# Kernel tuning notes

Hardware: AMD Instinct MI355X
Metric: run time of the kernel (lower is better)

The kernel has to match this reference:

```python
import jax, jax.numpy as jnp
import numpy as np

S = 5            # num_species
B = 1_000_000    # batch (proteins)
D = 32           # input_dim == hidden_dim (hard-coded 32 in forward)
EPS = 1e-5       # torch BatchNorm1d default eps
BRANCH_WEIGHT = 0.92


def setup_inputs() -> dict:
    key = jax.random.key(0)
    ks = jax.random.split(key, 20)
    f32 = jnp.float32
    inp = {
        "network_feat": jax.random.normal(ks[0], (B, D), f32),
        "species_ids": jax.random.randint(ks[1], (B,), 0, S),
        # per-species params, stacked along species axis. Weights stored [in, out]
        # (transpose of torch nn.Linear layout) so y = x @ W + b.
        "W1": jax.random.normal(ks[2], (S, D, D), f32) * 0.1,
        "b1": jax.random.normal(ks[3], (S, D), f32) * 0.1,
        "bn1_gamma": jax.random.uniform(ks[4], (S, D), f32, 0.5, 1.5),
        "bn1_beta": jax.random.normal(ks[5], (S, D), f32) * 0.1,
        "bn1_mean": jax.random.normal(ks[6], (S, D), f32) * 0.1,
        "bn1_var": jax.random.uniform(ks[7], (S, D), f32, 0.5, 1.5),
        "W2": jax.random.normal(ks[8], (S, D, D), f32) * 0.1,
        "b2": jax.random.normal(ks[9], (S, D), f32) * 0.1,
        "bn2_gamma": jax.random.uniform(ks[10], (S, D), f32, 0.5, 1.5),
        "bn2_beta": jax.random.normal(ks[11], (S, D), f32) * 0.1,
        "bn2_mean": jax.random.normal(ks[12], (S, D), f32) * 0.1,
        "bn2_var": jax.random.uniform(ks[13], (S, D), f32, 0.5, 1.5),
        "Wsc": jax.random.normal(ks[14], (S, D, D), f32) * 0.1,
        "bsc": jax.random.normal(ks[15], (S, D), f32) * 0.1,
        "Wsh": jax.random.normal(ks[16], (D, D), f32) * 0.1,
        "bsh": jax.random.normal(ks[17], (D,), f32) * 0.1,
    }
    return inp


def _bn(h, gamma, beta, mean, var):
    # BatchNorm1d in eval mode: running-stat normalization + affine.
    return (h - mean) * jax.lax.rsqrt(var + EPS) * gamma + beta


def reference(network_feat, species_ids, W1, b1, bn1_gamma, bn1_beta, bn1_mean,
              bn1_var, W2, b2, bn2_gamma, bn2_beta, bn2_mean, bn2_var,
              Wsc, bsc, Wsh, bsh):
    # Eval mode: dropout = identity, BN uses running stats.
    # Instead of gather/scatter per species, compute each species' tiny MLP on the
    # full batch and select with the species mask (same math; dense & fusible).
    x = network_feat
    out = jnp.zeros_like(x)
    for s in range(S):  # small fixed expert count
        shortcut = x @ Wsc[s] + bsc[s]
        h = jax.nn.relu(x @ W1[s] + b1[s])
        h = _bn(h, bn1_gamma[s], bn1_beta[s], bn1_mean[s], bn1_var[s])
        h = jax.nn.relu(h @ W2[s] + b2[s] + shortcut)
        h = _bn(h, bn2_gamma[s], bn2_beta[s], bn2_mean[s], bn2_var[s])
        mask = (species_ids == s)[:, None]  # [B, 1]
        out = jnp.where(mask, h, out)
    out = jax.nn.relu(out @ Wsh + bsh)  # shared MLP (dropout inactive)
    return out * BRANCH_WEIGHT
```

## Files before the change

kernel.cpp:

```cpp
#include <hip/hip_runtime.h>


#define EPSBN 1e-5f
#define TPB 256
#define WIN 256
#define NBLKMAX 768

typedef __attribute__((ext_vector_type(8))) short bf16x8;
typedef __attribute__((ext_vector_type(16))) float f32x16;
typedef __attribute__((ext_vector_type(4))) unsigned u32x4;

union FU { unsigned u[4]; bf16x8 v; u32x4 q; };

static __device__ __forceinline__ unsigned pkbf(float lo, float hi) {
    unsigned r;
    asm("v_cvt_pk_bf16_f32 %0, %1, %2" : "=v"(r) : "v"(lo), "v"(hi));
    return r;
}

static __device__ __forceinline__ void ldsbar() {
    asm volatile("s_waitcnt lgkmcnt(0)" ::: "memory");
    __builtin_amdgcn_s_barrier();
}

__global__ void k_pre(unsigned* __restrict__ wfrag, float* __restrict__ bconst,
                      const float* __restrict__ W1, const float* __restrict__ b1,
                      const float* __restrict__ g1, const float* __restrict__ be1,
                      const float* __restrict__ mu1, const float* __restrict__ va1,
                      const float* __restrict__ W2, const float* __restrict__ b2,
                      const float* __restrict__ g2, const float* __restrict__ be2,
                      const float* __restrict__ mu2, const float* __restrict__ va2,
                      const float* __restrict__ Wsc, const float* __restrict__ bsc,
                      const float* __restrict__ Wsh, const float* __restrict__ bsh) {
    if (blockIdx.x < 40) {
        const int i = blockIdx.x * 256 + threadIdx.x;
        const int p = i & 3, l = (i >> 2) & 63, c = (i >> 8) & 1;
        const int m = (i >> 9) & 3, s = i >> 11;
        const int ln = l & 31, hi = l >> 5;
        const int k0 = c * 16 + hi * 8 + 2 * p;
        float lo, hv;
        if (m == 0)      { lo = W1[s*1024 + k0*32 + ln];  hv = W1[s*1024 + (k0+1)*32 + ln]; }
        else if (m == 1) { lo = Wsc[s*1024 + k0*32 + ln]; hv = Wsc[s*1024 + (k0+1)*32 + ln]; }
        else if (m == 2) {
            float A0 = g1[s*32+k0]   * rsqrtf(va1[s*32+k0]   + EPSBN);
            float A1 = g1[s*32+k0+1] * rsqrtf(va1[s*32+k0+1] + EPSBN);
            lo = A0 * W2[s*1024 + k0*32 + ln]; hv = A1 * W2[s*1024 + (k0+1)*32 + ln];
        } else {
            float A0 = 0.92f * g2[s*32+k0]   * rsqrtf(va2[s*32+k0]   + EPSBN);
            float A1 = 0.92f * g2[s*32+k0+1] * rsqrtf(va2[s*32+k0+1] + EPSBN);
            lo = A0 * Wsh[k0*32 + ln]; hv = A1 * Wsh[(k0+1)*32 + ln];
        }
        wfrag[i] = pkbf(lo, hv);
    } else {
        for (int i = threadIdx.x; i < 480; i += 256) {
            const int reg = i & 15, hi = (i >> 4) & 1, t = i >> 5;
            const int q = t % 3, s = t / 3;
            const int r = (reg & 3) + 8 * (reg >> 2) + 4 * hi;
            float v;
            if (q == 0) v = b1[s*32 + r];
            else if (q == 1) {
                v = b2[s*32 + r] + bsc[s*32 + r];
                for (int k = 0; k < 32; ++k) {
                    float A = g1[s*32+k] * rsqrtf(va1[s*32+k] + EPSBN);
                    float C = be1[s*32+k] - mu1[s*32+k] * A;
                    v = fmaf(C, W2[s*1024 + k*32 + r], v);
                }
            } else {
                v = bsh[r];
                for (int k = 0; k < 32; ++k) {
                    float A = g2[s*32+k] * rsqrtf(va2[s*32+k] + EPSBN);
                    float C = be2[s*32+k] - mu2[s*32+k] * A;
                    v = fmaf(C, Wsh[k*32 + r], v);
                }
                v *= 0.92f;
            }
            bconst[i] = v;
        }
    }
}

static __device__ __forceinline__ void reluT(const f32x16& c, bf16x8& f0, bf16x8& f1) {
    unsigned p[8];
    #pragma unroll
    for (int i = 0; i < 8; ++i)
        p[i] = pkbf(fmaxf(c[2 * i], 0.f), fmaxf(c[2 * i + 1], 0.f));
    auto s0 = __builtin_amdgcn_permlane32_swap(p[0], p[2], false, false);
    auto s1 = __builtin_amdgcn_permlane32_swap(p[1], p[3], false, false);
    auto s2 = __builtin_amdgcn_permlane32_swap(p[4], p[6], false, false);
    auto s3 = __builtin_amdgcn_permlane32_swap(p[5], p[7], false, false);
    FU u0, u1;
    u0.u[0] = s0[0]; u0.u[1] = s1[0]; u0.u[2] = s0[1]; u0.u[3] = s1[1];
    u1.u[0] = s2[0]; u1.u[1] = s3[0]; u1.u[2] = s2[1]; u1.u[3] = s3[1];
    f0 = u0.v; f1 = u1.v;
}

__global__ __launch_bounds__(TPB, 3) void k_main(
    const float* __restrict__ X, const int* __restrict__ sid,
    const unsigned* __restrict__ wfrag, const float* __restrict__ bconst,
    float* __restrict__ out, int B) {
    __shared__ __align__(16) unsigned char xb[16384];
    __shared__ __align__(16) float ob[8192];
    __shared__ float clds[480];
    __shared__ int idxl[416];
    __shared__ int wq[4][5];

    const int tid = threadIdx.x;
    const int l   = tid & 63;
    const int ln  = l & 31;
    const int hi  = l >> 5;
    const int wav = tid >> 6;
    const unsigned long long ltmask = (1ull << l) - 1ull;

    for (int i = tid; i < 480; i += TPB) clds[i] = bconst[i];

    const int nwin = (B + WIN - 1) / WIN;
    const long fmaxo = (long)B * 32 - 8;

    float4 pa[4], pb[4];
    int svp = -1;

    int w0 = blockIdx.x;
    if (w0 < nwin) {
        #pragma unroll
        for (int k = 0; k < 4; ++k) {
            long fo = (long)w0 * (WIN * 32) + k * 2048 + tid * 8;
            if (fo > fmaxo) fo = fmaxo;
            pa[k] = *(const float4*)(X + fo);
            pb[k] = *(const float4*)(X + fo + 4);
        }
        int row = w0 * WIN + tid;
        svp = (row < B) ? sid[row < B ? row : B - 1] : -1;
    }

    for (int w = w0; w < nwin; w += gridDim.x) {
        const int wbase = w * WIN;
        const int rows = min(WIN, B - wbase);

        #pragma unroll
        for (int k = 0; k < 4; ++k) {
            FU u;
            u.u[0] = pkbf(pa[k].x, pa[k].y); u.u[1] = pkbf(pa[k].z, pa[k].w);
            u.u[2] = pkbf(pb[k].x, pb[k].y); u.u[3] = pkbf(pb[k].z, pb[k].w);
            const int row  = k * 64 + (tid >> 2);
            const int slot = (tid & 3) ^ (row & 3);
            *(u32x4*)(xb + row * 64 + slot * 16) = u.q;
        }

        const int s = svp;
        int prank = 0;
        #pragma unroll
        for (int sp = 0; sp < 5; ++sp) {
            unsigned long long m = __ballot(s == sp);
            if (l == 0) wq[wav][sp] = (int)__popcll(m);
            if (s == sp) prank = (int)__popcll(m & ltmask);
        }
        for (int i = tid; i < 416; i += TPB) idxl[i] = -1;
        ldsbar();

        int tb[6];
        {
            int t = 0;
            #pragma unroll
            for (int sp = 0; sp < 5; ++sp) {
                tb[sp] = t;
                int c = wq[0][sp] + wq[1][sp] + wq[2][sp] + wq[3][sp];
                t += (c + 31) >> 5;
            }
            tb[5] = t;
        }
        if (s >= 0) {
            int off = tb[s] * 32 + prank;
            for (int w2 = 0; w2 < wav; ++w2) off += wq[w2][s];
            idxl[off] = tid;
        }

        const int wn = w + gridDim.x;
        if (wn < nwin) {
            #pragma unroll
            for (int k = 0; k < 4; ++k) {
                long fo = (long)wn * (WIN * 32) + k * 2048 + tid * 8;
                if (fo > fmaxo) fo = fmaxo;
                pa[k] = *(const float4*)(X + fo);
                pb[k] = *(const float4*)(X + fo + 4);
            }
            int row = wn * WIN + tid;
            svp = (row < B) ? sid[row] : -1;
        }
        ldsbar();

        const int ntl = tb[5];
        for (int t = wav; t < ntl; t += 4) {
            int csp = 0;
            #pragma unroll
            for (int k = 1; k < 5; ++k) csp += (t >= tb[k]) ? 1 : 0;
            csp = __builtin_amdgcn_readfirstlane(csp);
            const int lid = idxl[t * 32 + ln];
            const int r = lid < 0 ? 0 : lid;

            const unsigned* wp = wfrag + csp * 2048;
            FU w00, w01, w10, w11, w20, w21, w30, w31;
            w00.q = *(const u32x4*)(wp + (0 * 64 + l) * 4);
            w01.q = *(const u32x4*)(wp + (1 * 64 + l) * 4);
            w10.q = *(const u32x4*)(wp + (2 * 64 + l) * 4);
            w11.q = *(const u32x4*)(wp + (3 * 64 + l) * 4);
            w20.q = *(const u32x4*)(wp + (4 * 64 + l) * 4);
            w21.q = *(const u32x4*)(wp + (5 * 64 + l) * 4);
            w30.q = *(const u32x4*)(wp + (6 * 64 + l) * 4);
            w31.q = *(const u32x4*)(wp + (7 * 64 + l) * 4);

            const float* cp = clds + csp * 96;
            f32x16 a1 = *(const f32x16*)(cp + hi * 16);
            f32x16 a2 = *(const f32x16*)(cp + 32 + hi * 16);

            const int rs = r & 3;
            const bf16x8 b0 = *(const bf16x8*)(xb + r * 64 + ((hi ^ rs) << 4));
            const bf16x8 b1 = *(const bf16x8*)(xb + r * 64 + (((2 + hi) ^ rs) << 4));

            a1 = __builtin_amdgcn_mfma_f32_32x32x16_bf16(w00.v, b0, a1, 0, 0, 0);
            a2 = __builtin_amdgcn_mfma_f32_32x32x16_bf16(w10.v, b0, a2, 0, 0, 0);
            a1 = __builtin_amdgcn_mfma_f32_32x32x16_bf16(w01.v, b1, a1, 0, 0, 0);
            a2 = __builtin_amdgcn_mfma_f32_32x32x16_bf16(w11.v, b1, a2, 0, 0, 0);

            bf16x8 h0, h1;
            reluT(a1, h0, h1);
            a2 = __builtin_amdgcn_mfma_f32_32x32x16_bf16(w20.v, h0, a2, 0, 0, 0);
            a2 = __builtin_amdgcn_mfma_f32_32x32x16_bf16(w21.v, h1, a2, 0, 0, 0);

            bf16x8 g0, g1;
            reluT(a2, g0, g1);
            f32x16 a3 = *(const f32x16*)(cp + 64 + hi * 16);
            a3 = __builtin_amdgcn_mfma_f32_32x32x16_bf16(w30.v, g0, a3, 0, 0, 0);
            a3 = __builtin_amdgcn_mfma_f32_32x32x16_bf16(w31.v, g1, a3, 0, 0, 0);

            if (lid >= 0) {
                #pragma unroll
                for (int q = 0; q < 4; ++q) {
                    float4 v;
                    v.x = fmaxf(a3[4 * q + 0], 0.f);
                    v.y = fmaxf(a3[4 * q + 1], 0.f);
                    v.z = fmaxf(a3[4 * q + 2], 0.f);
                    v.w = fmaxf(a3[4 * q + 3], 0.f);
                    const int fs = (hi * 4 + q * 8) ^ ((lid & 7) << 2);
                    *(float4*)(ob + lid * 32 + fs) = v;
                }
            }
        }
        ldsbar();

        #pragma unroll
        for (int k = 0; k < 8; ++k) {
            const int p = k * TPB + tid;
            const int row = p >> 3, sl = p & 7;
            if (row < rows) {
                const int fs = (sl * 4) ^ ((row & 7) << 2);
                float4 v = *(const float4*)(ob + row * 32 + fs);
                *(float4*)(out + (long)(wbase + row) * 32 + sl * 4) = v;
            }
        }
    }
}

extern "C" void kernel_launch(void* const* d_in, const int* in_sizes, int n_in,
                              void* d_out, int out_size, void* d_ws, size_t ws_size,
                              hipStream_t stream) {
    const float* X   = (const float*)d_in[0];
    const int*   sid = (const int*)d_in[1];
    const float* W1  = (const float*)d_in[2];
    const float* b1  = (const float*)d_in[3];
    const float* g1  = (const float*)d_in[4];
    const float* be1 = (const float*)d_in[5];
    const float* mu1 = (const float*)d_in[6];
    const float* va1 = (const float*)d_in[7];
    const float* W2  = (const float*)d_in[8];
    const float* b2  = (const float*)d_in[9];
    const float* g2  = (const float*)d_in[10];
    const float* be2 = (const float*)d_in[11];
    const float* mu2 = (const float*)d_in[12];
    const float* va2 = (const float*)d_in[13];
    const float* Wsc = (const float*)d_in[14];
    const float* bsc = (const float*)d_in[15];
    const float* Wsh = (const float*)d_in[16];
    const float* bsh = (const float*)d_in[17];
    float* out = (float*)d_out;
    const int B = in_sizes[1];

    unsigned* wfrag = (unsigned*)d_ws;
    float* bconst   = (float*)(wfrag + 10240);

    k_pre<<<41, 256, 0, stream>>>(wfrag, bconst,
                                  W1, b1, g1, be1, mu1, va1,
                                  W2, b2, g2, be2, mu2, va2,
                                  Wsc, bsc, Wsh, bsh);

    const int nwin = (B + WIN - 1) / WIN;
    const int nblocks = min(NBLKMAX, nwin);
    k_main<<<nblocks, TPB, 0, stream>>>(X, sid, wfrag, bconst, out, B);
}
```

Before: 63.66 us.

## Drop LDS output staging, store final MFMA results directly, raise occupancy

The last shared-MLP MFMA now swaps its operands so the result comes out transposed: each lane holds one output feature for 16 rows. The kernel writes straight to global memory using the row indices kept in LDS, which removes the 32KB output staging buffer and its barrier-and-copy phase. Freeing that LDS lets launch bounds rise from 3 to 5 blocks per SM and the grid cap rise to 1792 blocks. A per-species bias vector is added to the precomputed constants. The direct stores are scattered 4-byte writes: each lane writes to a different row, which may coalesce worse than the old float4 row copies.

```diff
diff --git a/kernel.cpp b/kernel.cpp
--- a/kernel.cpp
+++ b/kernel.cpp
@@ -4,7 +4,7 @@
 #define EPSBN 1e-5f
 #define TPB 256
 #define WIN 256
-#define NBLKMAX 768
+#define NBLKMAX 1792
 
 typedef __attribute__((ext_vector_type(8))) short bf16x8;
 typedef __attribute__((ext_vector_type(16))) float f32x16;
@@ -73,6 +73,7 @@
                     v = fmaf(C, Wsh[k*32 + r], v);
                 }
                 v *= 0.92f;
+                bconst[480 + s * 32 + r] = v;
             }
             bconst[i] = v;
         }
@@ -94,13 +95,12 @@
     f0 = u0.v; f1 = u1.v;
 }
 
-__global__ __launch_bounds__(TPB, 3) void k_main(
+__global__ __launch_bounds__(TPB, 5) void k_main(
     const float* __restrict__ X, const int* __restrict__ sid,
     const unsigned* __restrict__ wfrag, const float* __restrict__ bconst,
     float* __restrict__ out, int B) {
     __shared__ __align__(16) unsigned char xb[16384];
-    __shared__ __align__(16) float ob[8192];
-    __shared__ float clds[480];
+    __shared__ float clds[640];
     __shared__ int idxl[416];
     __shared__ int wq[4][5];
 
@@ -111,7 +111,7 @@
     const int wav = tid >> 6;
     const unsigned long long ltmask = (1ull << l) - 1ull;
 
-    for (int i = tid; i < 480; i += TPB) clds[i] = bconst[i];
+    for (int i = tid; i < 640; i += TPB) clds[i] = bconst[i];
 
     const int nwin = (B + WIN - 1) / WIN;
     const long fmaxo = (long)B * 32 - 8;
@@ -119,7 +119,7 @@
     float4 pa[4], pb[4];
     int svp = -1;
 
-    int w0 = blockIdx.x;
+    const int w0 = blockIdx.x;
     if (w0 < nwin) {
         #pragma unroll
         for (int k = 0; k < 4; ++k) {
@@ -128,13 +128,14 @@
             pa[k] = *(const float4*)(X + fo);
             pb[k] = *(const float4*)(X + fo + 4);
         }
-        int row = w0 * WIN + tid;
-        svp = (row < B) ? sid[row < B ? row : B - 1] : -1;
+        const int row = w0 * WIN + tid;
+        svp = (row < B) ? sid[row] : -1;
     }
 
     for (int w = w0; w < nwin; w += gridDim.x) {
         const int wbase = w * WIN;
-        const int rows = min(WIN, B - wbase);
+
+        ldsbar();
 
         #pragma unroll
         for (int k = 0; k < 4; ++k) {
@@ -183,7 +184,7 @@
                 pa[k] = *(const float4*)(X + fo);
                 pb[k] = *(const float4*)(X + fo + 4);
             }
-            int row = wn * WIN + tid;
+            const int row = wn * WIN + tid;
             svp = (row < B) ? sid[row] : -1;
         }
         ldsbar();
@@ -228,33 +229,20 @@
 
             bf16x8 g0, g1;
             reluT(a2, g0, g1);
-            f32x16 a3 = *(const f32x16*)(cp + 64 + hi * 16);
-            a3 = __builtin_amdgcn_mfma_f32_32x32x16_bf16(w30.v, g0, a3, 0, 0, 0);
-            a3 = __builtin_amdgcn_mfma_f32_32x32x16_bf16(w31.v, g1, a3, 0, 0, 0);
-
-            if (lid >= 0) {
-                #pragma unroll
-                for (int q = 0; q < 4; ++q) {
-                    float4 v;
-                    v.x = fmaxf(a3[4 * q + 0], 0.f);
-                    v.y = fmaxf(a3[4 * q + 1], 0.f);
-                    v.z = fmaxf(a3[4 * q + 2], 0.f);
-                    v.w = fmaxf(a3[4 * q + 3], 0.f);
-                    const int fs = (hi * 4 + q * 8) ^ ((lid & 7) << 2);
-                    *(float4*)(ob + lid * 32 + fs) = v;
-                }
-            }
-        }
-        ldsbar();
-
-        #pragma unroll
-        for (int k = 0; k < 8; ++k) {
-            const int p = k * TPB + tid;
-            const int row = p >> 3, sl = p & 7;
-            if (row < rows) {
-                const int fs = (sl * 4) ^ ((row & 7) << 2);
-                float4 v = *(const float4*)(ob + row * 32 + fs);
-                *(float4*)(out + (long)(wbase + row) * 32 + sl * 4) = v;
+
+            const float bsh_n = clds[480 + csp * 32 + ln];
+            f32x16 a3;
+            #pragma unroll
+            for (int rr = 0; rr < 16; ++rr) a3[rr] = bsh_n;
+            a3 = __builtin_amdgcn_mfma_f32_32x32x16_bf16(g0, w30.v, a3, 0, 0, 0);
+            a3 = __builtin_amdgcn_mfma_f32_32x32x16_bf16(g1, w31.v, a3, 0, 0, 0);
+
+            #pragma unroll
+            for (int reg = 0; reg < 16; ++reg) {
+                const int si = (reg & 3) + 8 * (reg >> 2) + 4 * hi;
+                const int lid2 = idxl[t * 32 + si];
+                if (lid2 >= 0)
+                    out[(long)(wbase + lid2) * 32 + ln] = fmaxf(a3[reg], 0.f);
             }
         }
     }
```

After: 111.4 us. 1.75x slower.

## Fuse weight preprocessing into main kernel, stage weights in LDS, bf16 output staging

Applied to the files above, without the earlier changes.

Removes the separate preprocessing kernel and has every block build the packed bf16 weight fragments and folded bias constants directly into shared memory. The per-tile weight fragment loads then come from LDS instead of global memory. Output staging in LDS switches from fp32 to packed bf16, and the grid shrinks to 512 blocks with 2 blocks per CU. This saves one kernel launch and its dependency, at the cost of redundant per-block preprocessing (including serial 32-step bias loops) and bf16 rounding of the final output.

```diff
diff --git a/kernel.cpp b/kernel.cpp
--- a/kernel.cpp
+++ b/kernel.cpp
@@ -4,11 +4,12 @@
 #define EPSBN 1e-5f
 #define TPB 256
 #define WIN 256
-#define NBLKMAX 768
+#define NBLK 512
 
 typedef __attribute__((ext_vector_type(8))) short bf16x8;
 typedef __attribute__((ext_vector_type(16))) float f32x16;
 typedef __attribute__((ext_vector_type(4))) unsigned u32x4;
+typedef __attribute__((ext_vector_type(2))) unsigned u32x2;
 
 union FU { unsigned u[4]; bf16x8 v; u32x4 q; };
 
@@ -21,62 +22,6 @@
 static __device__ __forceinline__ void ldsbar() {
     asm volatile("s_waitcnt lgkmcnt(0)" ::: "memory");
     __builtin_amdgcn_s_barrier();
-}
-
-__global__ void k_pre(unsigned* __restrict__ wfrag, float* __restrict__ bconst,
-                      const float* __restrict__ W1, const float* __restrict__ b1,
-                      const float* __restrict__ g1, const float* __restrict__ be1,
-                      const float* __restrict__ mu1, const float* __restrict__ va1,
-                      const float* __restrict__ W2, const float* __restrict__ b2,
-                      const float* __restrict__ g2, const float* __restrict__ be2,
-                      const float* __restrict__ mu2, const float* __restrict__ va2,
-                      const float* __restrict__ Wsc, const float* __restrict__ bsc,
-                      const float* __restrict__ Wsh, const float* __restrict__ bsh) {
-    if (blockIdx.x < 40) {
-        const int i = blockIdx.x * 256 + threadIdx.x;
-        const int p = i & 3, l = (i >> 2) & 63, c = (i >> 8) & 1;
-        const int m = (i >> 9) & 3, s = i >> 11;
-        const int ln = l & 31, hi = l >> 5;
-        const int k0 = c * 16 + hi * 8 + 2 * p;
-        float lo, hv;
-        if (m == 0)      { lo = W1[s*1024 + k0*32 + ln];  hv = W1[s*1024 + (k0+1)*32 + ln]; }
-        else if (m == 1) { lo = Wsc[s*1024 + k0*32 + ln]; hv = Wsc[s*1024 + (k0+1)*32 + ln]; }
-        else if (m == 2) {
-            float A0 = g1[s*32+k0]   * rsqrtf(va1[s*32+k0]   + EPSBN);
-            float A1 = g1[s*32+k0+1] * rsqrtf(va1[s*32+k0+1] + EPSBN);
-            lo = A0 * W2[s*1024 + k0*32 + ln]; hv = A1 * W2[s*1024 + (k0+1)*32 + ln];
-        } else {
-            float A0 = 0.92f * g2[s*32+k0]   * rsqrtf(va2[s*32+k0]   + EPSBN);
-            float A1 = 0.92f * g2[s*32+k0+1] * rsqrtf(va2[s*32+k0+1] + EPSBN);
-            lo = A0 * Wsh[k0*32 + ln]; hv = A1 * Wsh[(k0+1)*32 + ln];
-        }
-        wfrag[i] = pkbf(lo, hv);
-    } else {
-        for (int i = threadIdx.x; i < 480; i += 256) {
-            const int reg = i & 15, hi = (i >> 4) & 1, t = i >> 5;
-            const int q = t % 3, s = t / 3;
-            const int r = (reg & 3) + 8 * (reg >> 2) + 4 * hi;
-            float v;
-            if (q == 0) v = b1[s*32 + r];
-            else if (q == 1) {
-                v = b2[s*32 + r] + bsc[s*32 + r];
-                for (int k = 0; k < 32; ++k) {
-                    float A = g1[s*32+k] * rsqrtf(va1[s*32+k] + EPSBN);
-                    float C = be1[s*32+k] - mu1[s*32+k] * A;
-                    v = fmaf(C, W2[s*1024 + k*32 + r], v);
-                }
-            } else {
-                v = bsh[r];
-                for (int k = 0; k < 32; ++k) {
-                    float A = g2[s*32+k] * rsqrtf(va2[s*32+k] + EPSBN);
-                    float C = be2[s*32+k] - mu2[s*32+k] * A;
-                    v = fmaf(C, Wsh[k*32 + r], v);
-                }
-                v *= 0.92f;
-            }
-            bconst[i] = v;
-        }
-    }
 }
 
 static __device__ __forceinline__ void reluT(const f32x16& c, bf16x8& f0, bf16x8& f1) {
@@ -94,12 +39,20 @@
     f0 = u0.v; f1 = u1.v;
 }
 
-__global__ __launch_bounds__(TPB, 3) void k_main(
+__global__ __launch_bounds__(TPB, 2) void k_main(
     const float* __restrict__ X, const int* __restrict__ sid,
-    const unsigned* __restrict__ wfrag, const float* __restrict__ bconst,
+    const float* __restrict__ W1, const float* __restrict__ b1,
+    const float* __restrict__ g1, const float* __restrict__ be1,
+    const float* __restrict__ mu1, const float* __restrict__ va1,
+    const float* __restrict__ W2, const float* __restrict__ b2,
+    const float* __restrict__ g2, const float* __restrict__ be2,
+    const float* __restrict__ mu2, const float* __restrict__ va2,
+    const float* __restrict__ Wsc, const float* __restrict__ bsc,
+    const float* __restrict__ Wsh, const float* __restrict__ bsh,
     float* __restrict__ out, int B) {
+    __shared__ __align__(16) unsigned wlds[10240];
     __shared__ __align__(16) unsigned char xb[16384];
-    __shared__ __align__(16) float ob[8192];
+    __shared__ __align__(16) unsigned obh[4096];
     __shared__ float clds[480];
     __shared__ int idxl[416];
     __shared__ int wq[4][5];
@@ -111,15 +64,12 @@
     const int wav = tid >> 6;
     const unsigned long long ltmask = (1ull << l) - 1ull;
 
-    for (int i = tid; i < 480; i += TPB) clds[i] = bconst[i];
-
     const int nwin = (B + WIN - 1) / WIN;
     const long fmaxo = (long)B * 32 - 8;
 
     float4 pa[4], pb[4];
     int svp = -1;
-
-    int w0 = blockIdx.x;
+    const int w0 = blockIdx.x;
     if (w0 < nwin) {
         #pragma unroll
         for (int k = 0; k < 4; ++k) {
@@ -128,8 +78,52 @@
             pa[k] = *(const float4*)(X + fo);
             pb[k] = *(const float4*)(X + fo + 4);
         }
-        int row = w0 * WIN + tid;
-        svp = (row < B) ? sid[row < B ? row : B - 1] : -1;
+        const int row = w0 * WIN + tid;
+        svp = (row < B) ? sid[row] : -1;
+    }
+
+    for (int i = tid; i < 10240; i += TPB) {
+        const int p = i & 3, L = (i >> 2) & 63, c = (i >> 8) & 1;
+        const int m = (i >> 9) & 3, s = i >> 11;
+        const int LN = L & 31, HI = L >> 5;
+        const int k0 = c * 16 + HI * 8 + 2 * p;
+        float lo, hv;
+        if (m == 0)      { lo = W1[s*1024 + k0*32 + LN];  hv = W1[s*1024 + (k0+1)*32 + LN]; }
+        else if (m == 1) { lo = Wsc[s*1024 + k0*32 + LN]; hv = Wsc[s*1024 + (k0+1)*32 + LN]; }
+        else if (m == 2) {
+            float A0 = g1[s*32+k0]   * rsqrtf(va1[s*32+k0]   + EPSBN);
+            float A1 = g1[s*32+k0+1] * rsqrtf(va1[s*32+k0+1] + EPSBN);
+            lo = A0 * W2[s*1024 + k0*32 + LN]; hv = A1 * W2[s*1024 + (k0+1)*32 + LN];
+        } else {
+            float A0 = 0.92f * g2[s*32+k0]   * rsqrtf(va2[s*32+k0]   + EPSBN);
+            float A1 = 0.92f * g2[s*32+k0+1] * rsqrtf(va2[s*32+k0+1] + EPSBN);
+            lo = A0 * Wsh[k0*32 + LN]; hv = A1 * Wsh[(k0+1)*32 + LN];
+        }
+        wlds[i] = pkbf(lo, hv);
+    }
+    for (int i = tid; i < 480; i += TPB) {
+        const int reg = i & 15, HI = (i >> 4) & 1, t = i >> 5;
+        const int q = t % 3, s = t / 3;
+        const int r = (reg & 3) + 8 * (reg >> 2) + 4 * HI;
+        float v;
+        if (q == 0) v = b1[s*32 + r];
+        else if (q == 1) {
+            v = b2[s*32 + r] + bsc[s*32 + r];
+            for (int k = 0; k < 32; ++k) {
+                float A = g1[s*32+k] * rsqrtf(va1[s*32+k] + EPSBN);
+                float C = be1[s*32+k] - mu1[s*32+k] * A;
+                v = fmaf(C, W2[s*1024 + k*32 + r], v);
+            }
+        } else {
+            v = bsh[r];
+            for (int k = 0; k < 32; ++k) {
+                float A = g2[s*32+k] * rsqrtf(va2[s*32+k] + EPSBN);
+                float C = be2[s*32+k] - mu2[s*32+k] * A;
+                v = fmaf(C, Wsh[k*32 + r], v);
+            }
+            v *= 0.92f;
+        }
+        clds[i] = v;
     }
 
     for (int w = w0; w < nwin; w += gridDim.x) {
@@ -183,7 +177,7 @@
                 pa[k] = *(const float4*)(X + fo);
                 pb[k] = *(const float4*)(X + fo + 4);
             }
-            int row = wn * WIN + tid;
+            const int row = wn * WIN + tid;
             svp = (row < B) ? sid[row] : -1;
         }
         ldsbar();
@@ -197,7 +191,7 @@
             const int lid = idxl[t * 32 + ln];
             const int r = lid < 0 ? 0 : lid;
 
-            const unsigned* wp = wfrag + csp * 2048;
+            const unsigned* wp = wlds + csp * 2048;
             FU w00, w01, w10, w11, w20, w21, w30, w31;
             w00.q = *(const u32x4*)(wp + (0 * 64 + l) * 4);
             w01.q = *(const u32x4*)(wp + (1 * 64 + l) * 4);
@@ -235,13 +229,11 @@
             if (lid >= 0) {
                 #pragma unroll
                 for (int q = 0; q < 4; ++q) {
-                    float4 v;
-                    v.x = fmaxf(a3[4 * q + 0], 0.f);
-                    v.y = fmaxf(a3[4 * q + 1], 0.f);
-                    v.z = fmaxf(a3[4 * q + 2], 0.f);
-                    v.w = fmaxf(a3[4 * q + 3], 0.f);
-                    const int fs = (hi * 4 + q * 8) ^ ((lid & 7) << 2);
-                    *(float4*)(ob + lid * 32 + fs) = v;
+                    unsigned u0 = pkbf(fmaxf(a3[4 * q + 0], 0.f), fmaxf(a3[4 * q + 1], 0.f));
+                    unsigned u1 = pkbf(fmaxf(a3[4 * q + 2], 0.f), fmaxf(a3[4 * q + 3], 0.f));
+                    const int off = (4 * q + 2 * hi) ^ ((lid & 7) << 1);
+                    u32x2 uu; uu[0] = u0; uu[1] = u1;
+                    *(u32x2*)(obh + lid * 16 + off) = uu;
                 }
             }
         }
@@ -252,8 +244,13 @@
             const int p = k * TPB + tid;
             const int row = p >> 3, sl = p & 7;
             if (row < rows) {
-                const int fs = (sl * 4) ^ ((row & 7) << 2);
-                float4 v = *(const float4*)(ob + row * 32 + fs);
+                const int off = (sl * 2) ^ ((row & 7) << 1);
+                u32x2 uu = *(const u32x2*)(obh + row * 16 + off);
+                float4 v;
+                v.x = __uint_as_float(uu[0] << 16);
+                v.y = __uint_as_float(uu[0] & 0xffff0000u);
+                v.z = __uint_as_float(uu[1] << 16);
+                v.w = __uint_as_float(uu[1] & 0xffff0000u);
                 *(float4*)(out + (long)(wbase + row) * 32 + sl * 4) = v;
             }
         }
@@ -284,15 +281,10 @@
     float* out = (float*)d_out;
     const int B = in_sizes[1];
 
-    unsigned* wfrag = (unsigned*)d_ws;
-    float* bconst   = (float*)(wfrag + 10240);
-
-    k_pre<<<41, 256, 0, stream>>>(wfrag, bconst,
-                                  W1, b1, g1, be1, mu1, va1,
-                                  W2, b2, g2, be2, mu2, va2,
-                                  Wsc, bsc, Wsh, bsh);
-
     const int nwin = (B + WIN - 1) / WIN;
-    const int nblocks = min(NBLKMAX, nwin);
-    k_main<<<nblocks, TPB, 0, stream>>>(X, sid, wfrag, bconst, out, B);
-}
+    const int nblocks = min(NBLK, nwin);
+    k_main<<<nblocks, TPB, 0, stream>>>(X, sid,
+                                        W1, b1, g1, be1, mu1, va1,
+                                        W2, b2, g2, be2, mu2, va2,
+                                        Wsc, bsc, Wsh, bsh, out, B);
+}
```

Result: slower. 72.44 us (+13.8%).
